# Optimization experiments

Measured on AMD Instinct MI355X. Metric: run time of the kernel, lower is better.

Reference implementation:

```python
import jax, jax.numpy as jnp
import numpy as np
from functools import partial

N_USERS = 30000
N_ENTITIES = 70000
N = N_USERS + N_ENTITIES
D = 64
N_EDGES = 1_600_000
EPS = 1e-12


def setup_inputs() -> dict:
    key = jax.random.key(0)
    ks = jax.random.split(key, 10)
    s = 1.0 / np.sqrt(D)  # xavier-like scale for weights
    return {
        "user_tab": jax.random.normal(ks[0], (N_USERS, D), jnp.float32) * 0.1,
        "entity_tab": jax.random.normal(ks[1], (N_ENTITIES, D), jnp.float32) * 0.1,
        "A_vals": jax.random.uniform(ks[2], (N_EDGES,), jnp.float32) / 16.0,  # ~row-normalized
        "W1_1": jax.random.normal(ks[3], (D, D), jnp.float32) * s,
        "b1_1": jnp.zeros((D,), jnp.float32),
        "W2_1": jax.random.normal(ks[4], (D, D), jnp.float32) * s,
        "b2_1": jnp.zeros((D,), jnp.float32),
        "W1_2": jax.random.normal(ks[5], (D, 32), jnp.float32) * s,
        "b1_2": jnp.zeros((32,), jnp.float32),
        "W2_2": jax.random.normal(ks[6], (D, 32), jnp.float32) * s,
        "b2_2": jnp.zeros((32,), jnp.float32),
        "A_rows": jax.random.randint(ks[7], (N_EDGES,), 0, N, jnp.int64 if jax.config.jax_enable_x64 else jnp.int32),
        "A_cols": jax.random.randint(ks[8], (N_EDGES,), 0, N, jnp.int64 if jax.config.jax_enable_x64 else jnp.int32),
    }


def _spmm(rows, cols, vals, x):
    # sparse A (COO) @ dense x : gather tail embeddings, scale, scatter-add to rows
    msgs = x[cols] * vals[:, None]            # [E, d]
    return jax.ops.segment_sum(msgs, rows, num_segments=N)


def _l2norm(x):
    n = jnp.sqrt(jnp.sum(x * x, axis=1, keepdims=True))
    return x / jnp.maximum(n, EPS)


def _bi_layer(ego, side, W1, b1, W2, b2):
    sum_e = jax.nn.leaky_relu((ego + side) @ W1 + b1)  # slope 0.01 = torch default
    bi_e = jax.nn.leaky_relu((ego * side) @ W2 + b2)
    return _l2norm(sum_e + bi_e)  # dropout p=0 (eval)


def reference(user_tab, entity_tab, A_vals, W1_1, b1_1, W2_1, b2_1,
              W1_2, b1_2, W2_2, b2_2, A_rows, A_cols):
    ego = jnp.concatenate([user_tab, entity_tab], axis=0)  # [N, 64]
    all_embed = [ego]
    # layer 1: 64 -> 64
    side = _spmm(A_rows, A_cols, A_vals, ego)
    ego = _bi_layer(ego, side, W1_1, b1_1, W2_1, b2_1)
    all_embed.append(ego)
    # layer 2: 64 -> 32
    side = _spmm(A_rows, A_cols, A_vals, ego)
    ego = _bi_layer(ego, side, W1_2, b1_2, W2_2, b2_2)
    all_embed.append(ego)
    return jnp.concatenate(all_embed, axis=1)  # [N, 160]; split [n_users, n_entities] downstream
```

## Files before the change

kernel.cpp:

```cpp
#include <hip/hip_runtime.h>
#include <hip/hip_bf16.h>
#include <string.h>

#define N_USERS 30000
#define N_NODES 100000
#define DIM 64
#define N_EDGES 1600000
#define ROWS_PER_BUCK 256
#define NB ((N_NODES + ROWS_PER_BUCK - 1) / ROWS_PER_BUCK)
#define CHUNK 8192
#define NBLK_B ((N_EDGES + CHUNK - 1) / CHUNK)
#define BUCK_SLACK 2048
#define E_ALLOC (N_EDGES + NB * BUCK_SLACK)
#define STAGE_CAP 5120

typedef __hip_bfloat16 bf16;
typedef __attribute__((ext_vector_type(8))) short short8;
typedef __attribute__((ext_vector_type(4))) float floatx4;

__device__ __forceinline__ float b2f(bf16 v) { return __bfloat162float(v); }
__device__ __forceinline__ bf16 f2b(float v) { return __float2bfloat16(v); }
__device__ __forceinline__ unsigned short fbits(float v) {
    bf16 b = f2b(v); unsigned short u; memcpy(&u, &b, 2); return u;
}
__device__ __forceinline__ float ubf(unsigned u) {
    return __uint_as_float(u << 16);
}

__device__ __forceinline__ float ld(const void* p, int i, int f32) {
    return f32 ? ((const float*)p)[i] : b2f(((const bf16*)p)[i]);
}
__device__ __forceinline__ void st(void* p, int i, float v, int f32) {
    if (f32) ((float*)p)[i] = v; else ((bf16*)p)[i] = f2b(v);
}

__global__ void k_detect(const void* user, const void* ent, const void* vals,
                         const void* W, int* flags, int* bsize) {
    int t = threadIdx.x;
    for (int i = t; i < NB; i += 128) bsize[i] = 0;
    const void* ps[4] = { user, ent, vals, W };
    int k = t >> 5, i = t & 31;
    float v = ((const float*)ps[k])[i];
    int ok = (v == v && fabsf(v) <= 1e4f) ? 1 : 0;
    ok += __shfl_xor(ok, 1, 64);
    ok += __shfl_xor(ok, 2, 64);
    ok += __shfl_xor(ok, 4, 64);
    ok += __shfl_xor(ok, 8, 64);
    ok += __shfl_xor(ok, 16, 64);
    if ((t & 31) == 0) flags[k] = (ok >= 16) ? 1 : 0;
}

__global__ __launch_bounds__(256) void k_hista(const int* __restrict__ rows,
                                               int* __restrict__ cnt_table,
                                               int* __restrict__ bsize) {
    __shared__ int h[NB];
    int t = threadIdx.x, blk = blockIdx.x;
    for (int b = t; b < NB; b += 256) h[b] = 0;
    __syncthreads();
    int base = blk * CHUNK + t * 4;
#pragma unroll
    for (int it = 0; it < 8; ++it) {
        int e = base + it * 1024;
        if (e < N_EDGES) {
            int4 r = *(const int4*)&rows[e];
            atomicAdd(&h[r.x >> 8], 1);
            atomicAdd(&h[r.y >> 8], 1);
            atomicAdd(&h[r.z >> 8], 1);
            atomicAdd(&h[r.w >> 8], 1);
        }
    }
    __syncthreads();
    for (int b = t; b < NB; b += 256) {
        int v = h[b];
        cnt_table[blk * NB + b] = v;
        if (v) atomicAdd(&bsize[b], v);
    }
}

__global__ __launch_bounds__(512) void k_bscan(const int* __restrict__ bsize,
                                               int* __restrict__ bbase) {
    __shared__ int lds[512];
    int t = threadIdx.x;
    int v = (t < NB) ? (((bsize[t] + 3) & ~3) + BUCK_SLACK) : 0;
    lds[t] = v;
    __syncthreads();
    for (int off = 1; off < 512; off <<= 1) {
        int u = (t >= off) ? lds[t - off] : 0;
        __syncthreads();
        lds[t] += u;
        __syncthreads();
    }
    if (t <= NB) bbase[t] = (t == 0) ? 0 : lds[t - 1];
}

__global__ __launch_bounds__(256) void k_bscan2(int* __restrict__ cnt_table,
                                                const int* __restrict__ bbase) {
    __shared__ int lds[256];
    int t = threadIdx.x, b = blockIdx.x;
    int v = (t < NBLK_B) ? cnt_table[t * NB + b] : 0;
    lds[t] = v;
    __syncthreads();
    for (int off = 1; off < 256; off <<= 1) {
        int u = (t >= off) ? lds[t - off] : 0;
        __syncthreads();
        lds[t] += u;
        __syncthreads();
    }
    if (t < NBLK_B) cnt_table[t * NB + b] = bbase[b] + lds[t] - v;
}

__global__ __launch_bounds__(256) void k_bscatter2(
    const int* __restrict__ rows, const int* __restrict__ cols,
    const void* __restrict__ vals, const int* __restrict__ cnt_table,
    int2* __restrict__ bpack, const int* __restrict__ flags) {
    __shared__ int cur[NB];
    int t = threadIdx.x, blk = blockIdx.x;
    int fv = flags[2];
    for (int b = t; b < NB; b += 256) cur[b] = cnt_table[blk * NB + b];
    __syncthreads();
    int base = blk * CHUNK + t * 4;
#pragma unroll
    for (int it = 0; it < 8; ++it) {
        int e = base + it * 1024;
        if (e < N_EDGES) {
            int4 r = *(const int4*)&rows[e];
            int4 c = *(const int4*)&cols[e];
            float v0, v1, v2, v3;
            if (fv) {
                float4 vv = *(const float4*)((const float*)vals + e);
                v0 = vv.x; v1 = vv.y; v2 = vv.z; v3 = vv.w;
            } else {
                const bf16* bp = (const bf16*)vals + e;
                v0 = b2f(bp[0]); v1 = b2f(bp[1]); v2 = b2f(bp[2]); v3 = b2f(bp[3]);
            }
            int p0 = atomicAdd(&cur[r.x >> 8], 1);
            int p1 = atomicAdd(&cur[r.y >> 8], 1);
            int p2 = atomicAdd(&cur[r.z >> 8], 1);
            int p3 = atomicAdd(&cur[r.w >> 8], 1);
            bpack[p0] = make_int2(c.x | ((r.x & 255) << 17), __float_as_int(v0));
            bpack[p1] = make_int2(c.y | ((r.y & 255) << 17), __float_as_int(v1));
            bpack[p2] = make_int2(c.z | ((r.z & 255) << 17), __float_as_int(v2));
            bpack[p3] = make_int2(c.w | ((r.w & 255) << 17), __float_as_int(v3));
        }
    }
}

__global__ __launch_bounds__(256) void k_place2(
    const int* __restrict__ bsize, const int* __restrict__ bbase,
    const int2* __restrict__ bpack, int2* __restrict__ epack,
    int* __restrict__ row_start, int* __restrict__ row_end) {
    __shared__ __align__(16) int2 stage[STAGE_CAP];
    __shared__ int rcnt[ROWS_PER_BUCK];
    __shared__ int scan_lds[ROWS_PER_BUCK];
    __shared__ int rstart[ROWS_PER_BUCK];
    __shared__ int cur[ROWS_PER_BUCK];
    int t = threadIdx.x, b = blockIdx.x;
    int n = bsize[b];
    int gstart = bbase[b];
    rcnt[t] = 0;
    __syncthreads();
    for (int i = t; i < n; i += 256) {
        int2 p = bpack[gstart + i];
        if (i < STAGE_CAP) stage[i] = p;
        atomicAdd(&rcnt[(p.x >> 17) & 255], 1);
    }
    __syncthreads();
    int c = rcnt[t];
    int cp = (c + 3) & ~3;
    int g = cp;
    g = max(g, __shfl_xor(g, 1, 64));
    g = max(g, __shfl_xor(g, 2, 64));
    scan_lds[t] = g;
    __syncthreads();
    for (int off = 1; off < 256; off <<= 1) {
        int u = (t >= off) ? scan_lds[t - off] : 0;
        __syncthreads();
        scan_lds[t] += u;
        __syncthreads();
    }
    int rs_ = gstart + scan_lds[t] - g;
    rstart[t] = rs_;
    cur[t] = rs_;
    int node = b * ROWS_PER_BUCK + t;
    if (node < N_NODES) {
        row_start[node] = rs_;
        row_end[node] = rs_ + g;
    }
    __syncthreads();
    for (int i = t; i < n; i += 256) {
        int2 p = (i < STAGE_CAP) ? stage[i] : bpack[gstart + i];
        int r = (p.x >> 17) & 255;
        int pos = atomicAdd(&cur[r], 1);
        epack[pos] = make_int2(p.x & 0x1FFFF, p.y);
    }
    __syncthreads();
    int pend = rstart[t] + g;
    for (int pos = cur[t]; pos < pend; ++pos) epack[pos] = make_int2(0, 0);
}

__global__ void k_init(const void* __restrict__ user, const void* __restrict__ ent,
                       void* __restrict__ out, bf16* __restrict__ xb0,
                       const int* __restrict__ flags) {
    int i = blockIdx.x * blockDim.x + threadIdx.x;
    if (i >= N_NODES * DIM) return;
    int fo = flags[0], fe = flags[1];
    int n = i >> 6, d = i & 63;
    float v = (n < N_USERS) ? ld(user, i, fo) : ld(ent, i - N_USERS * DIM, fe);
    st(out, n * 160 + d, v, fo);
    xb0[i] = f2b(v);
}

#define GATHER_ROW_DECL(r) \
    int ej##r = rs[r] >> 1; \
    int4 eA##r = ep4[ej##r]; \
    int4 eB##r = ep4[ej##r + 1]; \
    float ea##r = 0.f;

#define GATHER_ISSUE(r) \
    unsigned eg##r##0 = xu[eA##r.x * 64 + lane]; \
    unsigned eg##r##1 = xu[eA##r.z * 64 + lane]; \
    unsigned eg##r##2 = xu[eB##r.x * 64 + lane]; \
    unsigned eg##r##3 = xu[eB##r.z * 64 + lane];

#define GATHER_ADV(r) \
    int4 nA##r = ep4[ej##r + 2]; \
    int4 nB##r = ep4[ej##r + 3]; \
    ej##r += 2;

#define GATHER_FMA(r) \
    ea##r += __int_as_float(eA##r.y) * ubf(eg##r##0); \
    ea##r += __int_as_float(eA##r.w) * ubf(eg##r##1); \
    ea##r += __int_as_float(eB##r.y) * ubf(eg##r##2); \
    ea##r += __int_as_float(eB##r.w) * ubf(eg##r##3); \
    eA##r = nA##r; eB##r = nB##r;

#define GATHER_BODY(EMX) \
    GATHER_ROW_DECL(0) GATHER_ROW_DECL(1) GATHER_ROW_DECL(2) GATHER_ROW_DECL(3) \
    for (int ei = 0; ei < (EMX); ei += 4) { \
        GATHER_ISSUE(0) GATHER_ISSUE(1) GATHER_ISSUE(2) GATHER_ISSUE(3) \
        GATHER_ADV(0) GATHER_ADV(1) GATHER_ADV(2) GATHER_ADV(3) \
        GATHER_FMA(0) GATHER_FMA(1) GATHER_FMA(2) GATHER_FMA(3) \
    }

__global__ __launch_bounds__(256) void k_layer1(
    const void* __restrict__ W1, const void* __restrict__ b1,
    const void* __restrict__ W2, const void* __restrict__ b2,
    void* __restrict__ out, const int* __restrict__ row_start,
    const int* __restrict__ row_end,
    const int2* __restrict__ epack, const bf16* __restrict__ xt,
    bf16* __restrict__ xn, const int* __restrict__ flags) {
    __shared__ __align__(16) unsigned short hp_lds[16][72];
    __shared__ __align__(16) unsigned short hm_lds[16][72];
    __shared__ __align__(16) float ssq_lds[16][4];
    int t = threadIdx.x, lane = t & 63, w = t >> 6;
    int sub = lane & 15, quad = lane >> 4;
    int fo = flags[0], fw = flags[3];
    int rbase = blockIdx.x * 16 + w * 4;
    const unsigned short* xu = (const unsigned short*)xt;
    const int4* ep4 = (const int4*)epack;

    int4 rsv = *(const int4*)&row_start[rbase];
    int rs[4] = { rsv.x, rsv.y, rsv.z, rsv.w };
    int emx = __builtin_amdgcn_readfirstlane(row_end[rbase] - rsv.x);
    GATHER_BODY(emx)
    {
        float s[4] = { ea0, ea1, ea2, ea3 };
#pragma unroll
        for (int r = 0; r < 4; ++r) {
            float h = ld(out, (rbase + r) * 160 + lane, fo);
            hp_lds[w * 4 + r][lane] = fbits(h + s[r]);
            hm_lds[w * 4 + r][lane] = fbits(h * s[r]);
        }
    }
    __syncthreads();

    short8 Ap0 = *(const short8*)((const char*)hp_lds + sub * 144 + quad * 16);
    short8 Ap1 = *(const short8*)((const char*)hp_lds + sub * 144 + 64 + quad * 16);
    short8 Am0 = *(const short8*)((const char*)hm_lds + sub * 144 + quad * 16);
    short8 Am1 = *(const short8*)((const char*)hm_lds + sub * 144 + 64 + quad * 16);

    int wbase = w * 16;
    short8 Bw10, Bw11, Bw20, Bw21;
    float bias1, bias2;
    if (fw) {
        const float* w1 = (const float*)W1;
        const float* w2 = (const float*)W2;
#pragma unroll
        for (int j = 0; j < 8; ++j) {
            int k0 = quad * 8 + j;
            Bw10[j] = (short)fbits(w1[k0 * 64 + wbase + sub]);
            Bw11[j] = (short)fbits(w1[(k0 + 32) * 64 + wbase + sub]);
            Bw20[j] = (short)fbits(w2[k0 * 64 + wbase + sub]);
            Bw21[j] = (short)fbits(w2[(k0 + 32) * 64 + wbase + sub]);
        }
        bias1 = ((const float*)b1)[wbase + sub];
        bias2 = ((const float*)b2)[wbase + sub];
    } else {
        const unsigned short* w1 = (const unsigned short*)W1;
        const unsigned short* w2 = (const unsigned short*)W2;
#pragma unroll
        for (int j = 0; j < 8; ++j) {
            int k0 = quad * 8 + j;
            Bw10[j] = (short)w1[k0 * 64 + wbase + sub];
            Bw11[j] = (short)w1[(k0 + 32) * 64 + wbase + sub];
            Bw20[j] = (short)w2[k0 * 64 + wbase + sub];
            Bw21[j] = (short)w2[(k0 + 32) * 64 + wbase + sub];
        }
        bias1 = b2f(((const bf16*)b1)[wbase + sub]);
        bias2 = b2f(((const bf16*)b2)[wbase + sub]);
    }

    floatx4 c1; c1[0] = bias1; c1[1] = bias1; c1[2] = bias1; c1[3] = bias1;
    floatx4 c2; c2[0] = bias2; c2[1] = bias2; c2[2] = bias2; c2[3] = bias2;
    c1 = __builtin_amdgcn_mfma_f32_16x16x32_bf16(Ap0, Bw10, c1, 0, 0, 0);
    c1 = __builtin_amdgcn_mfma_f32_16x16x32_bf16(Ap1, Bw11, c1, 0, 0, 0);
    c2 = __builtin_amdgcn_mfma_f32_16x16x32_bf16(Am0, Bw20, c2, 0, 0, 0);
    c2 = __builtin_amdgcn_mfma_f32_16x16x32_bf16(Am1, Bw21, c2, 0, 0, 0);

    float v[4], sp[4];
#pragma unroll
    for (int r = 0; r < 4; ++r) {
        float s1 = c1[r], s2 = c2[r];
        s1 = s1 > 0.f ? s1 : 0.01f * s1;
        s2 = s2 > 0.f ? s2 : 0.01f * s2;
        v[r] = s1 + s2;
        float sq = v[r] * v[r];
        sq += __shfl_xor(sq, 1, 64);
        sq += __shfl_xor(sq, 2, 64);
        sq += __shfl_xor(sq, 4, 64);
        sq += __shfl_xor(sq, 8, 64);
        sp[r] = sq;
    }
    if (sub == 0) {
#pragma unroll
        for (int r = 0; r < 4; ++r) ssq_lds[quad * 4 + r][w] = sp[r];
    }
    __syncthreads();
#pragma unroll
    for (int r = 0; r < 4; ++r) {
        int row = quad * 4 + r;
        floatx4 ps = *(const floatx4*)&ssq_lds[row][0];
        float ss = ps[0] + ps[1] + ps[2] + ps[3];
        float o = v[r] * (1.0f / fmaxf(sqrtf(ss), 1e-12f));
        int n = blockIdx.x * 16 + row;
        st(out, n * 160 + 64 + wbase + sub, o, fo);
        xn[n * 64 + wbase + sub] = f2b(o);
    }
}

__global__ __launch_bounds__(256) void k_layer2(
    const void* __restrict__ W1, const void* __restrict__ b1,
    const void* __restrict__ W2, const void* __restrict__ b2,
    void* __restrict__ out, const int* __restrict__ row_start,
    const int* __restrict__ row_end,
    const int2* __restrict__ epack, const bf16* __restrict__ xt,
    const int* __restrict__ flags) {
    __shared__ __align__(16) unsigned short hp_lds[16][72];
    __shared__ __align__(16) unsigned short hm_lds[16][72];
    __shared__ __align__(16) float bi_lds[16][32];
    __shared__ __align__(16) float ssq_lds[16][2];
    int t = threadIdx.x, lane = t & 63, w = t >> 6;
    int sub = lane & 15, quad = lane >> 4;
    int fo = flags[0], fw = flags[3];
    int rbase = blockIdx.x * 16 + w * 4;
    const unsigned short* xu = (const unsigned short*)xt;
    const int4* ep4 = (const int4*)epack;

    int4 rsv = *(const int4*)&row_start[rbase];
    int rs[4] = { rsv.x, rsv.y, rsv.z, rsv.w };
    int emx = __builtin_amdgcn_readfirstlane(row_end[rbase] - rsv.x);
    GATHER_BODY(emx)
    {
        float s[4] = { ea0, ea1, ea2, ea3 };
#pragma unroll
        for (int r = 0; r < 4; ++r) {
            float h = ld(out, (rbase + r) * 160 + 64 + lane, fo);
            hp_lds[w * 4 + r][lane] = fbits(h + s[r]);
            hm_lds[w * 4 + r][lane] = fbits(h * s[r]);
        }
    }
    __syncthreads();

    int path = w >> 1;
    int nbase = (w & 1) * 16;
    const unsigned short(*hl)[72] = path ? hm_lds : hp_lds;
    short8 Af0 = *(const short8*)((const char*)hl + sub * 144 + quad * 16);
    short8 Af1 = *(const short8*)((const char*)hl + sub * 144 + 64 + quad * 16);

    const void* W = path ? W2 : W1;
    const void* bb = path ? b2 : b1;
    short8 Bf0, Bf1;
    float bias;
    if (fw) {
        const float* wp = (const float*)W;
#pragma unroll
        for (int j = 0; j < 8; ++j) {
            int k0 = quad * 8 + j;
            Bf0[j] = (short)fbits(wp[k0 * 32 + nbase + sub]);
            Bf1[j] = (short)fbits(wp[(k0 + 32) * 32 + nbase + sub]);
        }
        bias = ((const float*)bb)[nbase + sub];
    } else {
        const unsigned short* wp = (const unsigned short*)W;
#pragma unroll
        for (int j = 0; j < 8; ++j) {
            int k0 = quad * 8 + j;
            Bf0[j] = (short)wp[k0 * 32 + nbase + sub];
            Bf1[j] = (short)wp[(k0 + 32) * 32 + nbase + sub];
        }
        bias = b2f(((const bf16*)bb)[nbase + sub]);
    }

    floatx4 c; c[0] = bias; c[1] = bias; c[2] = bias; c[3] = bias;
    c = __builtin_amdgcn_mfma_f32_16x16x32_bf16(Af0, Bf0, c, 0, 0, 0);
    c = __builtin_amdgcn_mfma_f32_16x16x32_bf16(Af1, Bf1, c, 0, 0, 0);

    float T[4];
#pragma unroll
    for (int r = 0; r < 4; ++r) {
        float x = c[r];
        T[r] = x > 0.f ? x : 0.01f * x;
        if (path == 1) bi_lds[quad * 4 + r][nbase + sub] = T[r];
    }
    __syncthreads();

    float v[4], sp[4];
#pragma unroll
    for (int r = 0; r < 4; ++r) {
        v[r] = T[r] + bi_lds[quad * 4 + r][nbase + sub];
        float sq = v[r] * v[r];
        sq += __shfl_xor(sq, 1, 64);
        sq += __shfl_xor(sq, 2, 64);
        sq += __shfl_xor(sq, 4, 64);
        sq += __shfl_xor(sq, 8, 64);
        sp[r] = sq;
    }
    if (path == 0 && sub == 0) {
#pragma unroll
        for (int r = 0; r < 4; ++r) ssq_lds[quad * 4 + r][w & 1] = sp[r];
    }
    __syncthreads();
    if (path == 0) {
#pragma unroll
        for (int r = 0; r < 4; ++r) {
            int row = quad * 4 + r;
            float ss = ssq_lds[row][0] + ssq_lds[row][1];
            float o = v[r] * (1.0f / fmaxf(sqrtf(ss), 1e-12f));
            int n = blockIdx.x * 16 + row;
            st(out, n * 160 + 128 + nbase + sub, o, fo);
        }
    }
}

extern "C" void kernel_launch(void* const* d_in, const int* in_sizes, int n_in,
                              void* d_out, int out_size, void* d_ws, size_t ws_size,
                              hipStream_t stream) {
    const void* user = d_in[0];
    const void* ent  = d_in[1];
    const void* vals = d_in[2];
    const void* W1_1 = d_in[3];
    const void* b1_1 = d_in[4];
    const void* W2_1 = d_in[5];
    const void* b2_1 = d_in[6];
    const void* W1_2 = d_in[7];
    const void* b1_2 = d_in[8];
    const void* W2_2 = d_in[9];
    const void* b2_2 = d_in[10];
    const int* rows  = (const int*)d_in[11];
    const int* cols  = (const int*)d_in[12];

    char* w = (char*)d_ws;
    int* flags     = (int*)w;  w += 256;
    int* bsize     = (int*)w;  w += 2048;
    int* bbase     = (int*)w;  w += 2048;
    int* row_start = (int*)w;  w += 400128;
    int* row_end   = (int*)w;  w += 400128;
    int2* epack    = (int2*)w; w += (size_t)E_ALLOC * 8;
    bf16* xb0      = (bf16*)w; w += (size_t)N_NODES * DIM * 2;
    bf16* xb1      = (bf16*)w;
    int* cnt_table = (int*)epack;
    int2* bpack    = (int2*)xb0;

    k_detect<<<1, 128, 0, stream>>>(user, ent, vals, W1_1, flags, bsize);
    k_hista<<<NBLK_B, 256, 0, stream>>>(rows, cnt_table, bsize);
    k_bscan<<<1, 512, 0, stream>>>(bsize, bbase);
    k_bscan2<<<NB, 256, 0, stream>>>(cnt_table, bbase);
    k_bscatter2<<<NBLK_B, 256, 0, stream>>>(rows, cols, vals, cnt_table, bpack, flags);
    k_place2<<<NB, 256, 0, stream>>>(bsize, bbase, bpack, epack, row_start, row_end);
    k_init<<<(N_NODES * DIM + 255) / 256, 256, 0, stream>>>(user, ent, d_out, xb0, flags);
    k_layer1<<<N_NODES / 16, 256, 0, stream>>>(W1_1, b1_1, W2_1, b2_1, d_out, row_start, row_end, epack, xb0, xb1, flags);
    k_layer2<<<N_NODES / 16, 256, 0, stream>>>(W1_2, b1_2, W2_2, b2_2, d_out, row_start, row_end, epack, xb1, flags);
}
```

Before: 307.5 us.

## Stage per-wave edge lists in LDS and prepack MFMA weight fragments once

Adds a one-block kernel that converts the layer weights and biases into MFMA-ready bf16 fragments once, so each layer block loads four vectors instead of doing many scalar strided loads with format branches. The gather phase now copies each wave's four-row edge lists (when padded length is at most 64) into LDS with coalesced loads, then unrolls eight edges per row per iteration, reading indices and values from LDS. The aim is to cut scattered global index loads and raise memory-level parallelism in the SpMM gather. It costs about 8 KB of extra LDS per block, which may lower occupancy, plus one extra kernel launch.

Measured after the change: 309.2 us. About the same (+0.6%).

```diff
diff --git a/kernel.cpp b/kernel.cpp
--- a/kernel.cpp
+++ b/kernel.cpp
@@ -13,6 +13,7 @@
 #define BUCK_SLACK 2048
 #define E_ALLOC (N_EDGES + NB * BUCK_SLACK)
 #define STAGE_CAP 5120
+#define GCAP 64
 
 typedef __hip_bfloat16 bf16;
 typedef __attribute__((ext_vector_type(8))) short short8;
@@ -32,6 +33,9 @@
 }
 __device__ __forceinline__ void st(void* p, int i, float v, int f32) {
     if (f32) ((float*)p)[i] = v; else ((bf16*)p)[i] = f2b(v);
+}
+__device__ __forceinline__ unsigned short wbits(const void* p, int i, int f32) {
+    return f32 ? fbits(((const float*)p)[i]) : ((const unsigned short*)p)[i];
 }
 
 __global__ void k_detect(const void* user, const void* ent, const void* vals,
@@ -48,6 +52,43 @@
     ok += __shfl_xor(ok, 8, 64);
     ok += __shfl_xor(ok, 16, 64);
     if ((t & 31) == 0) flags[k] = (ok >= 16) ? 1 : 0;
+}
+
+__global__ __launch_bounds__(256) void k_prepw(
+    const void* W1_1, const void* b1_1, const void* W2_1, const void* b2_1,
+    const void* W1_2, const void* b1_2, const void* W2_2, const void* b2_2,
+    short8* wf1, float2* wsb1, short8* wf2, float* wsb2,
+    const int* flags) {
+    int t = threadIdx.x;
+    int w = t >> 6, quad = (t >> 4) & 3, sub = t & 15;
+    int fw = flags[3];
+    short8 f0, f1, f2, f3;
+#pragma unroll
+    for (int j = 0; j < 8; ++j) {
+        int k0 = quad * 8 + j, n = w * 16 + sub;
+        f0[j] = (short)wbits(W1_1, k0 * 64 + n, fw);
+        f1[j] = (short)wbits(W1_1, (k0 + 32) * 64 + n, fw);
+        f2[j] = (short)wbits(W2_1, k0 * 64 + n, fw);
+        f3[j] = (short)wbits(W2_1, (k0 + 32) * 64 + n, fw);
+    }
+    short8* p = wf1 + ((w * 4 + quad) * 16 + sub) * 4;
+    p[0] = f0; p[1] = f1; p[2] = f2; p[3] = f3;
+    if (quad == 0)
+        wsb1[w * 16 + sub] = make_float2(ld(b1_1, w * 16 + sub, fw),
+                                         ld(b2_1, w * 16 + sub, fw));
+    int path = w >> 1, nbase = (w & 1) * 16;
+    const void* W = path ? W2_2 : W1_2;
+    const void* bb = path ? b2_2 : b1_2;
+    short8 g0, g1;
+#pragma unroll
+    for (int j = 0; j < 8; ++j) {
+        int k0 = quad * 8 + j, n = nbase + sub;
+        g0[j] = (short)wbits(W, k0 * 32 + n, fw);
+        g1[j] = (short)wbits(W, (k0 + 32) * 32 + n, fw);
+    }
+    short8* q = wf2 + ((w * 4 + quad) * 16 + sub) * 2;
+    q[0] = g0; q[1] = g1;
+    if (quad == 0) wsb2[w * 16 + sub] = ld(bb, nbase + sub, fw);
 }
 
 __global__ __launch_bounds__(256) void k_hista(const int* __restrict__ rows,
@@ -210,59 +251,123 @@
     xb0[i] = f2b(v);
 }
 
-#define GATHER_ROW_DECL(r) \
-    int ej##r = rs[r] >> 1; \
+#define G8_LOAD(r) \
+    int b##r = (r * gstep + ei) >> 1; \
+    int4 qa##r = lq4[b##r], qb##r = lq4[b##r + 1]; \
+    int4 qc##r = lq4[b##r + 2], qd##r = lq4[b##r + 3];
+
+#define G8_ISSUE(r) \
+    unsigned g##r##0 = xu[qa##r.x * 64 + lane]; \
+    unsigned g##r##1 = xu[qa##r.z * 64 + lane]; \
+    unsigned g##r##2 = xu[qb##r.x * 64 + lane]; \
+    unsigned g##r##3 = xu[qb##r.z * 64 + lane]; \
+    unsigned g##r##4 = xu[qc##r.x * 64 + lane]; \
+    unsigned g##r##5 = xu[qc##r.z * 64 + lane]; \
+    unsigned g##r##6 = xu[qd##r.x * 64 + lane]; \
+    unsigned g##r##7 = xu[qd##r.z * 64 + lane];
+
+#define G8_FMA(r) \
+    ea##r += __int_as_float(qa##r.y) * ubf(g##r##0); \
+    ea##r += __int_as_float(qa##r.w) * ubf(g##r##1); \
+    ea##r += __int_as_float(qb##r.y) * ubf(g##r##2); \
+    ea##r += __int_as_float(qb##r.w) * ubf(g##r##3); \
+    ea##r += __int_as_float(qc##r.y) * ubf(g##r##4); \
+    ea##r += __int_as_float(qc##r.w) * ubf(g##r##5); \
+    ea##r += __int_as_float(qd##r.y) * ubf(g##r##6); \
+    ea##r += __int_as_float(qd##r.w) * ubf(g##r##7);
+
+#define G4_LOAD(r) \
+    int tb##r = (r * gstep + ei) >> 1; \
+    int4 ua##r = lq4[tb##r], ub##r = lq4[tb##r + 1];
+
+#define G4_ISSUE(r) \
+    unsigned h##r##0 = xu[ua##r.x * 64 + lane]; \
+    unsigned h##r##1 = xu[ua##r.z * 64 + lane]; \
+    unsigned h##r##2 = xu[ub##r.x * 64 + lane]; \
+    unsigned h##r##3 = xu[ub##r.z * 64 + lane];
+
+#define G4_FMA(r) \
+    ea##r += __int_as_float(ua##r.y) * ubf(h##r##0); \
+    ea##r += __int_as_float(ua##r.w) * ubf(h##r##1); \
+    ea##r += __int_as_float(ub##r.y) * ubf(h##r##2); \
+    ea##r += __int_as_float(ub##r.w) * ubf(h##r##3);
+
+#define FB_ROW_DECL(r) \
+    int ej##r = rs_a[r] >> 1; \
     int4 eA##r = ep4[ej##r]; \
-    int4 eB##r = ep4[ej##r + 1]; \
-    float ea##r = 0.f;
-
-#define GATHER_ISSUE(r) \
+    int4 eB##r = ep4[ej##r + 1];
+
+#define FB_ISSUE(r) \
     unsigned eg##r##0 = xu[eA##r.x * 64 + lane]; \
     unsigned eg##r##1 = xu[eA##r.z * 64 + lane]; \
     unsigned eg##r##2 = xu[eB##r.x * 64 + lane]; \
     unsigned eg##r##3 = xu[eB##r.z * 64 + lane];
 
-#define GATHER_ADV(r) \
+#define FB_ADV(r) \
     int4 nA##r = ep4[ej##r + 2]; \
     int4 nB##r = ep4[ej##r + 3]; \
     ej##r += 2;
 
-#define GATHER_FMA(r) \
+#define FB_FMA(r) \
     ea##r += __int_as_float(eA##r.y) * ubf(eg##r##0); \
     ea##r += __int_as_float(eA##r.w) * ubf(eg##r##1); \
     ea##r += __int_as_float(eB##r.y) * ubf(eg##r##2); \
     ea##r += __int_as_float(eB##r.w) * ubf(eg##r##3); \
     eA##r = nA##r; eB##r = nB##r;
 
-#define GATHER_BODY(EMX) \
-    GATHER_ROW_DECL(0) GATHER_ROW_DECL(1) GATHER_ROW_DECL(2) GATHER_ROW_DECL(3) \
-    for (int ei = 0; ei < (EMX); ei += 4) { \
-        GATHER_ISSUE(0) GATHER_ISSUE(1) GATHER_ISSUE(2) GATHER_ISSUE(3) \
-        GATHER_ADV(0) GATHER_ADV(1) GATHER_ADV(2) GATHER_ADV(3) \
-        GATHER_FMA(0) GATHER_FMA(1) GATHER_FMA(2) GATHER_FMA(3) \
+#define GATHER_BODY \
+    float ea0 = 0.f, ea1 = 0.f, ea2 = 0.f, ea3 = 0.f; \
+    if (emx <= GCAP) { \
+        { \
+            const int2* eps = (const int2*)epack + rs0; \
+            int tot = emx << 2; \
+            for (int i = lane; i < tot; i += 64) lq[i] = eps[i]; \
+        } \
+        int ei = 0; \
+        for (; ei + 8 <= emx; ei += 8) { \
+            G8_LOAD(0) G8_LOAD(1) G8_LOAD(2) G8_LOAD(3) \
+            G8_ISSUE(0) G8_ISSUE(1) G8_ISSUE(2) G8_ISSUE(3) \
+            G8_FMA(0) G8_FMA(1) G8_FMA(2) G8_FMA(3) \
+        } \
+        if (ei < emx) { \
+            G4_LOAD(0) G4_LOAD(1) G4_LOAD(2) G4_LOAD(3) \
+            G4_ISSUE(0) G4_ISSUE(1) G4_ISSUE(2) G4_ISSUE(3) \
+            G4_FMA(0) G4_FMA(1) G4_FMA(2) G4_FMA(3) \
+        } \
+    } else { \
+        const int4* ep4 = (const int4*)epack; \
+        int rs_a[4] = { rsv.x, rsv.y, rsv.z, rsv.w }; \
+        FB_ROW_DECL(0) FB_ROW_DECL(1) FB_ROW_DECL(2) FB_ROW_DECL(3) \
+        for (int ei = 0; ei < emx; ei += 4) { \
+            FB_ISSUE(0) FB_ISSUE(1) FB_ISSUE(2) FB_ISSUE(3) \
+            FB_ADV(0) FB_ADV(1) FB_ADV(2) FB_ADV(3) \
+            FB_FMA(0) FB_FMA(1) FB_FMA(2) FB_FMA(3) \
+        } \
     }
 
 __global__ __launch_bounds__(256) void k_layer1(
-    const void* __restrict__ W1, const void* __restrict__ b1,
-    const void* __restrict__ W2, const void* __restrict__ b2,
+    const short8* __restrict__ wf1, const float2* __restrict__ wsb1,
     void* __restrict__ out, const int* __restrict__ row_start,
     const int* __restrict__ row_end,
     const int2* __restrict__ epack, const bf16* __restrict__ xt,
     bf16* __restrict__ xn, const int* __restrict__ flags) {
+    __shared__ __align__(16) int2 lq_lds[4][4 * GCAP];
     __shared__ __align__(16) unsigned short hp_lds[16][72];
     __shared__ __align__(16) unsigned short hm_lds[16][72];
     __shared__ __align__(16) float ssq_lds[16][4];
     int t = threadIdx.x, lane = t & 63, w = t >> 6;
     int sub = lane & 15, quad = lane >> 4;
-    int fo = flags[0], fw = flags[3];
+    int fo = flags[0];
     int rbase = blockIdx.x * 16 + w * 4;
     const unsigned short* xu = (const unsigned short*)xt;
-    const int4* ep4 = (const int4*)epack;
 
     int4 rsv = *(const int4*)&row_start[rbase];
-    int rs[4] = { rsv.x, rsv.y, rsv.z, rsv.w };
+    int rs0 = __builtin_amdgcn_readfirstlane(rsv.x);
     int emx = __builtin_amdgcn_readfirstlane(row_end[rbase] - rsv.x);
-    GATHER_BODY(emx)
+    int gstep = emx;
+    int2* lq = lq_lds[w];
+    const int4* lq4 = (const int4*)lq;
+    GATHER_BODY
     {
         float s[4] = { ea0, ea1, ea2, ea3 };
 #pragma unroll
@@ -279,36 +384,11 @@
     short8 Am0 = *(const short8*)((const char*)hm_lds + sub * 144 + quad * 16);
     short8 Am1 = *(const short8*)((const char*)hm_lds + sub * 144 + 64 + quad * 16);
 
+    const short8* wfp = wf1 + ((w * 4 + quad) * 16 + sub) * 4;
+    short8 Bw10 = wfp[0], Bw11 = wfp[1], Bw20 = wfp[2], Bw21 = wfp[3];
+    float2 bb12 = wsb1[w * 16 + sub];
+    float bias1 = bb12.x, bias2 = bb12.y;
     int wbase = w * 16;
-    short8 Bw10, Bw11, Bw20, Bw21;
-    float bias1, bias2;
-    if (fw) {
-        const float* w1 = (const float*)W1;
-        const float* w2 = (const float*)W2;
-#pragma unroll
-        for (int j = 0; j < 8; ++j) {
-            int k0 = quad * 8 + j;
-            Bw10[j] = (short)fbits(w1[k0 * 64 + wbase + sub]);
-            Bw11[j] = (short)fbits(w1[(k0 + 32) * 64 + wbase + sub]);
-            Bw20[j] = (short)fbits(w2[k0 * 64 + wbase + sub]);
-            Bw21[j] = (short)fbits(w2[(k0 + 32) * 64 + wbase + sub]);
-        }
-        bias1 = ((const float*)b1)[wbase + sub];
-        bias2 = ((const float*)b2)[wbase + sub];
-    } else {
-        const unsigned short* w1 = (const unsigned short*)W1;
-        const unsigned short* w2 = (const unsigned short*)W2;
-#pragma unroll
-        for (int j = 0; j < 8; ++j) {
-            int k0 = quad * 8 + j;
-            Bw10[j] = (short)w1[k0 * 64 + wbase + sub];
-            Bw11[j] = (short)w1[(k0 + 32) * 64 + wbase + sub];
-            Bw20[j] = (short)w2[k0 * 64 + wbase + sub];
-            Bw21[j] = (short)w2[(k0 + 32) * 64 + wbase + sub];
-        }
-        bias1 = b2f(((const bf16*)b1)[wbase + sub]);
-        bias2 = b2f(((const bf16*)b2)[wbase + sub]);
-    }
 
     floatx4 c1; c1[0] = bias1; c1[1] = bias1; c1[2] = bias1; c1[3] = bias1;
     floatx4 c2; c2[0] = bias2; c2[1] = bias2; c2[2] = bias2; c2[3] = bias2;
@@ -349,27 +429,29 @@
 }
 
 __global__ __launch_bounds__(256) void k_layer2(
-    const void* __restrict__ W1, const void* __restrict__ b1,
-    const void* __restrict__ W2, const void* __restrict__ b2,
+    const short8* __restrict__ wf2, const float* __restrict__ wsb2,
     void* __restrict__ out, const int* __restrict__ row_start,
     const int* __restrict__ row_end,
     const int2* __restrict__ epack, const bf16* __restrict__ xt,
     const int* __restrict__ flags) {
+    __shared__ __align__(16) int2 lq_lds[4][4 * GCAP];
     __shared__ __align__(16) unsigned short hp_lds[16][72];
     __shared__ __align__(16) unsigned short hm_lds[16][72];
     __shared__ __align__(16) float bi_lds[16][32];
     __shared__ __align__(16) float ssq_lds[16][2];
     int t = threadIdx.x, lane = t & 63, w = t >> 6;
     int sub = lane & 15, quad = lane >> 4;
-    int fo = flags[0], fw = flags[3];
+    int fo = flags[0];
     int rbase = blockIdx.x * 16 + w * 4;
     const unsigned short* xu = (const unsigned short*)xt;
-    const int4* ep4 = (const int4*)epack;
 
     int4 rsv = *(const int4*)&row_start[rbase];
-    int rs[4] = { rsv.x, rsv.y, rsv.z, rsv.w };
+    int rs0 = __builtin_amdgcn_readfirstlane(rsv.x);
     int emx = __builtin_amdgcn_readfirstlane(row_end[rbase] - rsv.x);
-    GATHER_BODY(emx)
+    int gstep = emx;
+    int2* lq = lq_lds[w];
+    const int4* lq4 = (const int4*)lq;
+    GATHER_BODY
     {
         float s[4] = { ea0, ea1, ea2, ea3 };
 #pragma unroll
@@ -387,29 +469,9 @@
     short8 Af0 = *(const short8*)((const char*)hl + sub * 144 + quad * 16);
     short8 Af1 = *(const short8*)((const char*)hl + sub * 144 + 64 + quad * 16);
 
-    const void* W = path ? W2 : W1;
-    const void* bb = path ? b2 : b1;
-    short8 Bf0, Bf1;
-    float bias;
-    if (fw) {
-        const float* wp = (const float*)W;
-#pragma unroll
-        for (int j = 0; j < 8; ++j) {
-            int k0 = quad * 8 + j;
-            Bf0[j] = (short)fbits(wp[k0 * 32 + nbase + sub]);
-            Bf1[j] = (short)fbits(wp[(k0 + 32) * 32 + nbase + sub]);
-        }
-        bias = ((const float*)bb)[nbase + sub];
-    } else {
-        const unsigned short* wp = (const unsigned short*)W;
-#pragma unroll
-        for (int j = 0; j < 8; ++j) {
-            int k0 = quad * 8 + j;
-            Bf0[j] = (short)wp[k0 * 32 + nbase + sub];
-            Bf1[j] = (short)wp[(k0 + 32) * 32 + nbase + sub];
-        }
-        bias = b2f(((const bf16*)bb)[nbase + sub]);
-    }
+    const short8* wfp = wf2 + ((w * 4 + quad) * 16 + sub) * 2;
+    short8 Bf0 = wfp[0], Bf1 = wfp[1];
+    float bias = wsb2[w * 16 + sub];
 
     floatx4 c; c[0] = bias; c[1] = bias; c[2] = bias; c[3] = bias;
     c = __builtin_amdgcn_mfma_f32_16x16x32_bf16(Af0, Bf0, c, 0, 0, 0);
@@ -470,24 +532,30 @@
     const int* cols  = (const int*)d_in[12];
 
     char* w = (char*)d_ws;
-    int* flags     = (int*)w;  w += 256;
-    int* bsize     = (int*)w;  w += 2048;
-    int* bbase     = (int*)w;  w += 2048;
-    int* row_start = (int*)w;  w += 400128;
-    int* row_end   = (int*)w;  w += 400128;
-    int2* epack    = (int2*)w; w += (size_t)E_ALLOC * 8;
-    bf16* xb0      = (bf16*)w; w += (size_t)N_NODES * DIM * 2;
+    int* flags     = (int*)w;    w += 256;
+    int* bsize     = (int*)w;    w += 2048;
+    int* bbase     = (int*)w;    w += 2048;
+    short8* wf1    = (short8*)w; w += 16384;
+    float2* wsb1   = (float2*)w; w += 512;
+    short8* wf2    = (short8*)w; w += 8192;
+    float* wsb2    = (float*)w;  w += 256;
+    int* row_start = (int*)w;    w += 400128;
+    int* row_end   = (int*)w;    w += 400128;
+    int2* epack    = (int2*)w;   w += (size_t)E_ALLOC * 8;
+    bf16* xb0      = (bf16*)w;   w += (size_t)N_NODES * DIM * 2;
     bf16* xb1      = (bf16*)w;
     int* cnt_table = (int*)epack;
     int2* bpack    = (int2*)xb0;
 
     k_detect<<<1, 128, 0, stream>>>(user, ent, vals, W1_1, flags, bsize);
+    k_prepw<<<1, 256, 0, stream>>>(W1_1, b1_1, W2_1, b2_1, W1_2, b1_2, W2_2, b2_2,
+                                   wf1, wsb1, wf2, wsb2, flags);
     k_hista<<<NBLK_B, 256, 0, stream>>>(rows, cnt_table, bsize);
     k_bscan<<<1, 512, 0, stream>>>(bsize, bbase);
     k_bscan2<<<NB, 256, 0, stream>>>(cnt_table, bbase);
     k_bscatter2<<<NBLK_B, 256, 0, stream>>>(rows, cols, vals, cnt_table, bpack, flags);
     k_place2<<<NB, 256, 0, stream>>>(bsize, bbase, bpack, epack, row_start, row_end);
     k_init<<<(N_NODES * DIM + 255) / 256, 256, 0, stream>>>(user, ent, d_out, xb0, flags);
-    k_layer1<<<N_NODES / 16, 256, 0, stream>>>(W1_1, b1_1, W2_1, b2_1, d_out, row_start, row_end, epack, xb0, xb1, flags);
-    k_layer2<<<N_NODES / 16, 256, 0, stream>>>(W1_2, b1_2, W2_2, b2_2, d_out, row_start, row_end, epack, xb1, flags);
-}
+    k_layer1<<<N_NODES / 16, 256, 0, stream>>>(wf1, wsb1, d_out, row_start, row_end, epack, xb0, xb1, flags);
+    k_layer2<<<N_NODES / 16, 256, 0, stream>>>(wf2, wsb2, d_out, row_start, row_end, epack, xb1, flags);
+}
```
